# Kernel optimization log

Hardware: AMD Instinct MI355X
Metric: run time of the kernel (lower is better)

## Reference

```python
import jax, jax.numpy as jnp
import numpy as np

D_MODEL, N_HEADS, D_K, D_V = 512, 8, 32, 32
LN_EPS = 1e-5


def setup_inputs() -> dict:
    key = jax.random.key(0)
    ks = jax.random.split(key, 12)
    B, L = 4, 2048
    inner = N_HEADS * D_K
    s_in = 1.0 / np.sqrt(D_MODEL)
    s_fc = 1.0 / np.sqrt(inner)
    return {
        "q": jax.random.normal(ks[0], (B, L, D_MODEL), jnp.float32),
        "k": jax.random.normal(ks[1], (B, L, D_MODEL), jnp.float32),
        "v": jax.random.normal(ks[2], (B, L, D_MODEL), jnp.float32),
        "Wq": jax.random.normal(ks[3], (inner, D_MODEL), jnp.float32) * s_in,
        "bq": jax.random.normal(ks[4], (inner,), jnp.float32) * 0.01,
        "Wk": jax.random.normal(ks[5], (inner, D_MODEL), jnp.float32) * s_in,
        "bk": jax.random.normal(ks[6], (inner,), jnp.float32) * 0.01,
        "Wv": jax.random.normal(ks[7], (N_HEADS * D_V, D_MODEL), jnp.float32) * s_in,
        "bv": jax.random.normal(ks[8], (N_HEADS * D_V,), jnp.float32) * 0.01,
        "Wfc": jax.random.normal(ks[9], (D_MODEL, N_HEADS * D_V), jnp.float32) * s_fc,
        "bfc": jax.random.normal(ks[10], (D_MODEL,), jnp.float32) * 0.01,
        "gamma": jnp.ones((D_MODEL,), jnp.float32),
        "beta": jnp.zeros((D_MODEL,), jnp.float32),
    }


def reference(q, k, v, Wq, bq, Wk, bk, Wv, bv, Wfc, bfc, gamma, beta):
    n, l, _ = q.shape
    # Projection output interpreted as (..., d_k, n_heads): head idx is fastest dim
    def split_heads(x, W, b, dh):
        p = x @ W.T + b                     # [n, l, dh*H]
        return p.reshape(n, x.shape[1], dh, N_HEADS).transpose(0, 3, 1, 2)  # [n,H,l,dh]

    qh = split_heads(q, Wq, bq, D_K)
    kh = split_heads(k, Wk, bk, D_K)
    vh = split_heads(v, Wv, bv, D_V)

    scale = 1.0 / jnp.sqrt(jnp.asarray(D_K, q.dtype))
    scores = jnp.einsum('nhqd,nhkd->nhqk', qh, kh) * scale  # [n,H,L,L]
    att = jax.nn.softmax(scores, axis=-1)
    out = jnp.einsum('nhqk,nhkd->nhqd', att, vh)             # [n,H,L,d_v]
    out = out.transpose(0, 2, 1, 3).reshape(n, l, N_HEADS * D_V)

    fc = out @ Wfc.T + bfc
    x = fc + q  # residual
    mean = jnp.mean(x, axis=-1, keepdims=True)
    var = jnp.mean(jnp.square(x - mean), axis=-1, keepdims=True)
    return gamma * (x - mean) / jnp.sqrt(var + LN_EPS) + beta
```

## Files before the change

### kernel.cpp

```cpp
#include <hip/hip_runtime.h>
#include <math.h>

constexpr int Bn = 4, Ln = 2048, DM = 512, NH = 8, DKv = 32, INNER = 256;
constexpr int TTOK = Bn * Ln;
constexpr size_t HEAD_ELEMS = (size_t)Bn * NH * Ln * DKv;


typedef short short8 __attribute__((ext_vector_type(8)));
typedef short short4v __attribute__((ext_vector_type(4)));
typedef float floatx4 __attribute__((ext_vector_type(4)));

constexpr size_t XB_OFF  = 8u * 1024 * 1024;
constexpr size_t WB_OFF  = 12536832;
constexpr size_t WFCB_OFF = WB_OFF + 3 * 131072;

__device__ inline short f2bf(float x) {
  unsigned u = __builtin_bit_cast(unsigned, x);
  unsigned r = (u + 0x7FFFu + ((u >> 16) & 1u)) >> 16;
  return (short)r;
}

#if __has_builtin(__builtin_amdgcn_mfma_f32_16x16x16bf16_1k)
#define MFMA16(a, b, c) __builtin_amdgcn_mfma_f32_16x16x16bf16_1k(a, b, c, 0, 0, 0)
#else
__device__ inline floatx4 mfma16_asm(short4v a, short4v b, floatx4 c) {
  asm volatile("v_mfma_f32_16x16x16_bf16 %0, %1, %2, %3\n\ts_nop 4"
               : "=v"(c) : "v"(a), "v"(b), "0"(c));
  return c;
}
#define MFMA16(a, b, c) mfma16_asm(a, b, c)
#endif

__global__ __launch_bounds__(256) void cvtw_kernel(
    const float* __restrict__ Wq, const float* __restrict__ Wk,
    const float* __restrict__ Wv, const float* __restrict__ Wfc,
    short* __restrict__ Wb, short* __restrict__ Wfcb)
{
  const int z = blockIdx.y;
  const float* src = z == 0 ? Wq : (z == 1 ? Wk : (z == 2 ? Wv : Wfc));
  short* dst = z < 3 ? Wb + (size_t)z * 131072 : Wfcb;
  const int idx = (blockIdx.x * 256 + threadIdx.x) * 4;
  float4 x = *(const float4*)&src[idx];
  *(short4v*)&dst[idx] = (short4v){f2bf(x.x), f2bf(x.y), f2bf(x.z), f2bf(x.w)};
}

__global__ __launch_bounds__(256) void proj_kernel(
    const float* __restrict__ q, const float* __restrict__ k, const float* __restrict__ v,
    const short* __restrict__ Wb,
    const float* __restrict__ bq, const float* __restrict__ bk,
    const float* __restrict__ bv,
    short* __restrict__ ws)
{
  const int mat = blockIdx.z;
  const float* X    = mat == 0 ? q  : (mat == 1 ? k  : v);
  const short* W    = Wb + (size_t)mat * 131072;
  const float* bias = mat == 0 ? bq : (mat == 1 ? bk : bv);
  short* outp = ws + (size_t)mat * HEAD_ELEMS;

  const int t0 = blockIdx.x * 64;
  const int c0 = blockIdx.y * 64;
  const int tid = threadIdx.x;
  const int col = tid & 15;
  const int quad = (tid & 63) >> 4;
  const int w = tid >> 6;

  __shared__ short Xs[64 * 136];
  __shared__ short Wsh[64 * 136];

  floatx4 acc[4];
#pragma unroll
  for (int nj = 0; nj < 4; ++nj) acc[nj] = (floatx4){0.f, 0.f, 0.f, 0.f};

  float4 xr[8];
  short8 wr[4];
  auto loadX = [&](int k0) {
#pragma unroll
    for (int j = 0; j < 8; ++j) {
      const int i = tid + j * 256, row = i >> 5, c4 = i & 31;
      xr[j] = *(const float4*)&X[(size_t)(t0 + row) * DM + k0 + c4 * 4];
    }
  };
  auto loadW = [&](int k0) {
#pragma unroll
    for (int j = 0; j < 4; ++j) {
      const int s = tid + j * 256, row = s >> 4, k8 = s & 15;
      wr[j] = *(const short8*)&W[(size_t)(c0 + row) * DM + k0 + k8 * 8];
    }
  };

  loadX(0);
  loadW(0);

  for (int kc = 0; kc < 4; ++kc) {
#pragma unroll
    for (int j = 0; j < 8; ++j) {
      const int i = tid + j * 256, row = i >> 5, c4 = i & 31;
      *(short4v*)&Xs[row * 136 + c4 * 4] =
          (short4v){f2bf(xr[j].x), f2bf(xr[j].y), f2bf(xr[j].z), f2bf(xr[j].w)};
    }
#pragma unroll
    for (int j = 0; j < 4; ++j) {
      const int s = tid + j * 256, row = s >> 4, k8 = s & 15;
      *(short8*)&Wsh[row * 136 + k8 * 8] = wr[j];
    }
    __syncthreads();
    if (kc < 3) {
      loadX((kc + 1) * 128);
      loadW((kc + 1) * 128);
    }
#pragma unroll
    for (int ks = 0; ks < 4; ++ks) {
      short8 a = *(const short8*)&Xs[(w * 16 + col) * 136 + ks * 32 + quad * 8];
#pragma unroll
      for (int nj = 0; nj < 4; ++nj) {
        short8 b = *(const short8*)&Wsh[(nj * 16 + col) * 136 + ks * 32 + quad * 8];
        acc[nj] = __builtin_amdgcn_mfma_f32_16x16x32_bf16(a, b, acc[nj], 0, 0, 0);
      }
    }
    __syncthreads();
  }

#pragma unroll
  for (int nj = 0; nj < 4; ++nj) {
#pragma unroll
    for (int r = 0; r < 4; ++r) {
      const int t = t0 + w * 16 + quad * 4 + r;
      const int n = t >> 11, ll = t & (Ln - 1);
      const int c = c0 + nj * 16 + col;
      const int d = c >> 3, h = c & 7;
      const short val = f2bf(acc[nj][r] + bias[c]);
      if (mat < 2)
        outp[((size_t)(n * NH + h) * Ln + ll) * DKv + d] = val;
      else
        outp[((size_t)(n * NH + h) * DKv + d) * Ln + ll] = val;
    }
  }
}

__global__ __launch_bounds__(256) void attn_kernel(const short* __restrict__ ws,
                                                   short* __restrict__ O2b)
{
  const int bh = blockIdx.y;
  const int n = bh >> 3, h = bh & 7;
  const int tid = threadIdx.x;
  const int col = tid & 15;
  const int quad = (tid & 63) >> 4;
  const int w = tid >> 6;
  const int qi = blockIdx.x * 64 + w * 16 + col;

  const short* Qh = ws;
  const short* Kg = ws + HEAD_ELEMS + (size_t)bh * Ln * DKv;
  const short* Vg = ws + 2 * HEAD_ELEMS + (size_t)bh * DKv * Ln;

  __shared__ short Ks[64 * 32];
  __shared__ short Vs[32 * 72];

  const short8 aq = *(const short8*)&Qh[(size_t)bh * Ln * DKv + (size_t)qi * DKv + quad * 8];

  const float c1 = 0.25505654f;
  float lsum = 0.f;
  floatx4 o[2];
  o[0] = (floatx4){0.f, 0.f, 0.f, 0.f};
  o[1] = (floatx4){0.f, 0.f, 0.f, 0.f};

  const int vd = tid >> 3, vkb = tid & 7;
  short8 kr = *(const short8*)(Kg + tid * 8);
  short8 vr = *(const short8*)(Vg + (size_t)vd * Ln + vkb * 8);

  for (int kt = 0; kt < 32; ++kt) {
    *(short8*)&Ks[tid * 8] = kr;
    *(short8*)&Vs[vd * 72 + vkb * 8] = vr;
    __syncthreads();
    if (kt < 31) {
      kr = *(const short8*)(Kg + (size_t)(kt + 1) * 2048 + tid * 8);
      vr = *(const short8*)(Vg + (size_t)vd * Ln + (kt + 1) * 64 + vkb * 8);
    }

    floatx4 s[4];
    const floatx4 z4 = {0.f, 0.f, 0.f, 0.f};
#pragma unroll
    for (int ks = 0; ks < 4; ++ks) {
      short8 kf = *(const short8*)&Ks[(ks * 16 + col) * 32 + quad * 8];
      s[ks] = __builtin_amdgcn_mfma_f32_16x16x32_bf16(kf, aq, z4, 0, 0, 0);
    }

    short4v pf[4];
#pragma unroll
    for (int ks = 0; ks < 4; ++ks) {
      float p0 = __builtin_amdgcn_exp2f(s[ks][0] * c1);
      float p1 = __builtin_amdgcn_exp2f(s[ks][1] * c1);
      float p2 = __builtin_amdgcn_exp2f(s[ks][2] * c1);
      float p3 = __builtin_amdgcn_exp2f(s[ks][3] * c1);
      lsum += (p0 + p1) + (p2 + p3);
      unsigned u0 = __builtin_amdgcn_perm(__builtin_bit_cast(unsigned, p1),
                                          __builtin_bit_cast(unsigned, p0), 0x07060302u);
      unsigned u1 = __builtin_amdgcn_perm(__builtin_bit_cast(unsigned, p3),
                                          __builtin_bit_cast(unsigned, p2), 0x07060302u);
      uint2 uu = make_uint2(u0, u1);
      pf[ks] = __builtin_bit_cast(short4v, uu);
    }

#pragma unroll
    for (int ks = 0; ks < 4; ++ks) {
      short4v va0 = *(const short4v*)&Vs[col * 72 + ks * 16 + quad * 4];
      short4v va1 = *(const short4v*)&Vs[(16 + col) * 72 + ks * 16 + quad * 4];
      o[0] = MFMA16(va0, pf[ks], o[0]);
      o[1] = MFMA16(va1, pf[ks], o[1]);
    }
    __syncthreads();
  }

  lsum += __shfl_xor(lsum, 16);
  lsum += __shfl_xor(lsum, 32);
  const float inv = 1.f / lsum;

  short* dst = &O2b[((size_t)n * Ln + qi) * INNER + h * DKv];
#pragma unroll
  for (int dt = 0; dt < 2; ++dt)
#pragma unroll
    for (int r = 0; r < 4; ++r)
      dst[dt * 16 + quad * 4 + r] = f2bf(o[dt][r] * inv);
}

__global__ __launch_bounds__(256) void fc_kernel(
    const short* __restrict__ O2b, const short* __restrict__ Wfcb,
    const float* __restrict__ bfc, const float* __restrict__ qin,
    short* __restrict__ Xb)
{
  const int t0 = blockIdx.x * 64;
  const int c0 = blockIdx.y * 64;
  const int tid = threadIdx.x;
  const int col = tid & 15;
  const int quad = (tid & 63) >> 4;
  const int w = tid >> 6;

  __shared__ short As[64 * 264];
  __shared__ short Bs[64 * 264];

  for (int i = tid; i < 2048; i += 256) {
    const int row = i >> 5, k8 = i & 31;
    *(short8*)&As[row * 264 + k8 * 8] =
        *(const short8*)&O2b[(size_t)(t0 + row) * INNER + k8 * 8];
    *(short8*)&Bs[row * 264 + k8 * 8] =
        *(const short8*)&Wfcb[(size_t)(c0 + row) * INNER + k8 * 8];
  }
  __syncthreads();

  floatx4 acc[4];
#pragma unroll
  for (int nj = 0; nj < 4; ++nj) acc[nj] = (floatx4){0.f, 0.f, 0.f, 0.f};

#pragma unroll
  for (int ks = 0; ks < 8; ++ks) {
    short8 a = *(const short8*)&As[(w * 16 + col) * 264 + ks * 32 + quad * 8];
#pragma unroll
    for (int nj = 0; nj < 4; ++nj) {
      short8 b = *(const short8*)&Bs[(nj * 16 + col) * 264 + ks * 32 + quad * 8];
      acc[nj] = __builtin_amdgcn_mfma_f32_16x16x32_bf16(a, b, acc[nj], 0, 0, 0);
    }
  }

#pragma unroll
  for (int nj = 0; nj < 4; ++nj) {
#pragma unroll
    for (int r = 0; r < 4; ++r) {
      const int t = t0 + w * 16 + quad * 4 + r;
      const int c = c0 + nj * 16 + col;
      Xb[(size_t)t * DM + c] = f2bf(acc[nj][r] + bfc[c] + qin[(size_t)t * DM + c]);
    }
  }
}

__global__ __launch_bounds__(256) void ln_kernel(
    const short* __restrict__ Xb, const float* __restrict__ gamma,
    const float* __restrict__ beta, float* __restrict__ outp)
{
  const int t = blockIdx.x * 4 + (threadIdx.x >> 6);
  const int lane = threadIdx.x & 63;

  short8 xs = *(const short8*)&Xb[(size_t)t * DM + lane * 8];
  float x[8];
#pragma unroll
  for (int j = 0; j < 8; ++j)
    x[j] = __builtin_bit_cast(float, ((unsigned)(unsigned short)xs[j]) << 16);

  float s1 = 0.f, s2 = 0.f;
#pragma unroll
  for (int j = 0; j < 8; ++j) { s1 += x[j]; s2 += x[j] * x[j]; }
#pragma unroll
  for (int off = 32; off >= 1; off >>= 1) {
    s1 += __shfl_xor(s1, off);
    s2 += __shfl_xor(s2, off);
  }
  const float mean = s1 * (1.f / 512.f);
  const float var = s2 * (1.f / 512.f) - mean * mean;
  const float rstd = rsqrtf(var + 1e-5f);

  float4 g0 = *(const float4*)&gamma[lane * 8];
  float4 g1 = *(const float4*)&gamma[lane * 8 + 4];
  float4 b0 = *(const float4*)&beta[lane * 8];
  float4 b1 = *(const float4*)&beta[lane * 8 + 4];

  float4 y0, y1;
  y0.x = g0.x * (x[0] - mean) * rstd + b0.x;
  y0.y = g0.y * (x[1] - mean) * rstd + b0.y;
  y0.z = g0.z * (x[2] - mean) * rstd + b0.z;
  y0.w = g0.w * (x[3] - mean) * rstd + b0.w;
  y1.x = g1.x * (x[4] - mean) * rstd + b1.x;
  y1.y = g1.y * (x[5] - mean) * rstd + b1.y;
  y1.z = g1.z * (x[6] - mean) * rstd + b1.z;
  y1.w = g1.w * (x[7] - mean) * rstd + b1.w;

  float* drow = &outp[(size_t)t * DM + lane * 8];
  *(float4*)&drow[0] = y0;
  *(float4*)&drow[4] = y1;
}

extern "C" void kernel_launch(void* const* d_in, const int* in_sizes, int n_in,
                              void* d_out, int out_size, void* d_ws, size_t ws_size,
                              hipStream_t stream) {
  const float* q     = (const float*)d_in[0];
  const float* k     = (const float*)d_in[1];
  const float* v     = (const float*)d_in[2];
  const float* Wq    = (const float*)d_in[3];
  const float* bq    = (const float*)d_in[4];
  const float* Wk    = (const float*)d_in[5];
  const float* bk    = (const float*)d_in[6];
  const float* Wv    = (const float*)d_in[7];
  const float* bv    = (const float*)d_in[8];
  const float* Wfc   = (const float*)d_in[9];
  const float* bfc   = (const float*)d_in[10];
  const float* gamma = (const float*)d_in[11];
  const float* beta  = (const float*)d_in[12];

  short* wsS  = (short*)d_ws;
  short* O2b  = wsS + 3 * HEAD_ELEMS;
  short* Xb   = wsS + XB_OFF;
  short* Wb   = wsS + WB_OFF;
  short* Wfcb = wsS + WFCB_OFF;

  cvtw_kernel<<<dim3(128, 4), 256, 0, stream>>>(Wq, Wk, Wv, Wfc, Wb, Wfcb);

  dim3 gp(TTOK / 64, INNER / 64, 3);
  proj_kernel<<<gp, 256, 0, stream>>>(q, k, v, Wb, bq, bk, bv, wsS);

  dim3 gatt(Ln / 64, Bn * NH);
  attn_kernel<<<gatt, 256, 0, stream>>>(wsS, O2b);

  dim3 gfc(TTOK / 64, DM / 64);
  fc_kernel<<<gfc, 256, 0, stream>>>(O2b, Wfcb, bfc, q, Xb);

  ln_kernel<<<TTOK / 4, 256, 0, stream>>>(Xb, gamma, beta, (float*)d_out);
}
```

Baseline: 190.6 us.

## Double-buffer attention K/V tiles, pre-swizzle V in LDS, fold softmax scale into Q

The attention kernel now ping-pongs between two LDS buffers for K and V, which drops the trailing barrier in each tile iteration. V is written to shared memory in a permuted layout so each lane fetches both MFMA A-operands for a k-step with one 16-byte read. The softmax scale constant moves into the Q projection epilogue, removing a multiply per score. Pre-scaling Q before bf16 rounding changes numerics slightly, and the doubled LDS footprint may reduce occupancy.

```diff
diff --git a/kernel.cpp b/kernel.cpp
--- a/kernel.cpp
+++ b/kernel.cpp
@@ -13,6 +13,8 @@
 constexpr size_t XB_OFF  = 8u * 1024 * 1024;
 constexpr size_t WB_OFF  = 12536832;
 constexpr size_t WFCB_OFF = WB_OFF + 3 * 131072;
+
+constexpr float C1 = 0.25505654f;
 
 __device__ inline short f2bf(float x) {
   unsigned u = __builtin_bit_cast(unsigned, x);
@@ -128,7 +130,9 @@
       const int n = t >> 11, ll = t & (Ln - 1);
       const int c = c0 + nj * 16 + col;
       const int d = c >> 3, h = c & 7;
-      const short val = f2bf(acc[nj][r] + bias[c]);
+      float pv = acc[nj][r] + bias[c];
+      if (mat == 0) pv *= C1;
+      const short val = f2bf(pv);
       if (mat < 2)
         outp[((size_t)(n * NH + h) * Ln + ll) * DKv + d] = val;
       else
@@ -152,24 +156,29 @@
   const short* Kg = ws + HEAD_ELEMS + (size_t)bh * Ln * DKv;
   const short* Vg = ws + 2 * HEAD_ELEMS + (size_t)bh * DKv * Ln;
 
-  __shared__ short Ks[64 * 32];
-  __shared__ short Vs[32 * 72];
+  __shared__ short Ks[2][64 * 32];
+  __shared__ short Vs[2][64 * 32];
 
   const short8 aq = *(const short8*)&Qh[(size_t)bh * Ln * DKv + (size_t)qi * DKv + quad * 8];
 
-  const float c1 = 0.25505654f;
   float lsum = 0.f;
   floatx4 o[2];
   o[0] = (floatx4){0.f, 0.f, 0.f, 0.f};
   o[1] = (floatx4){0.f, 0.f, 0.f, 0.f};
 
   const int vd = tid >> 3, vkb = tid & 7;
+  const int voff1 = (vkb >> 1) * 512 + ((2 * vkb) & 3) * 128 + (vd & 15) * 8 + (vd >> 4) * 4;
+  const int voff2 = (vkb >> 1) * 512 + ((2 * vkb + 1) & 3) * 128 + (vd & 15) * 8 + (vd >> 4) * 4;
+
   short8 kr = *(const short8*)(Kg + tid * 8);
   short8 vr = *(const short8*)(Vg + (size_t)vd * Ln + vkb * 8);
 
   for (int kt = 0; kt < 32; ++kt) {
-    *(short8*)&Ks[tid * 8] = kr;
-    *(short8*)&Vs[vd * 72 + vkb * 8] = vr;
+    short* ksb = Ks[kt & 1];
+    short* vsb = Vs[kt & 1];
+    *(short8*)&ksb[tid * 8] = kr;
+    *(short4v*)&vsb[voff1] = __builtin_shufflevector(vr, vr, 0, 1, 2, 3);
+    *(short4v*)&vsb[voff2] = __builtin_shufflevector(vr, vr, 4, 5, 6, 7);
     __syncthreads();
     if (kt < 31) {
       kr = *(const short8*)(Kg + (size_t)(kt + 1) * 2048 + tid * 8);
@@ -180,17 +189,17 @@
     const floatx4 z4 = {0.f, 0.f, 0.f, 0.f};
 #pragma unroll
     for (int ks = 0; ks < 4; ++ks) {
-      short8 kf = *(const short8*)&Ks[(ks * 16 + col) * 32 + quad * 8];
+      short8 kf = *(const short8*)&ksb[(ks * 16 + col) * 32 + quad * 8];
       s[ks] = __builtin_amdgcn_mfma_f32_16x16x32_bf16(kf, aq, z4, 0, 0, 0);
     }
 
     short4v pf[4];
 #pragma unroll
     for (int ks = 0; ks < 4; ++ks) {
-      float p0 = __builtin_amdgcn_exp2f(s[ks][0] * c1);
-      float p1 = __builtin_amdgcn_exp2f(s[ks][1] * c1);
-      float p2 = __builtin_amdgcn_exp2f(s[ks][2] * c1);
-      float p3 = __builtin_amdgcn_exp2f(s[ks][3] * c1);
+      float p0 = __builtin_amdgcn_exp2f(s[ks][0]);
+      float p1 = __builtin_amdgcn_exp2f(s[ks][1]);
+      float p2 = __builtin_amdgcn_exp2f(s[ks][2]);
+      float p3 = __builtin_amdgcn_exp2f(s[ks][3]);
       lsum += (p0 + p1) + (p2 + p3);
       unsigned u0 = __builtin_amdgcn_perm(__builtin_bit_cast(unsigned, p1),
                                           __builtin_bit_cast(unsigned, p0), 0x07060302u);
@@ -202,12 +211,10 @@
 
 #pragma unroll
     for (int ks = 0; ks < 4; ++ks) {
-      short4v va0 = *(const short4v*)&Vs[col * 72 + ks * 16 + quad * 4];
-      short4v va1 = *(const short4v*)&Vs[(16 + col) * 72 + ks * 16 + quad * 4];
-      o[0] = MFMA16(va0, pf[ks], o[0]);
-      o[1] = MFMA16(va1, pf[ks], o[1]);
-    }
-    __syncthreads();
+      short8 vv = *(const short8*)&vsb[ks * 512 + quad * 128 + col * 8];
+      o[0] = MFMA16(__builtin_shufflevector(vv, vv, 0, 1, 2, 3), pf[ks], o[0]);
+      o[1] = MFMA16(__builtin_shufflevector(vv, vv, 4, 5, 6, 7), pf[ks], o[1]);
+    }
   }
 
   lsum += __shfl_xor(lsum, 16);
```

Measured after the change: 194.2 us. Within noise of the previous version (+1.9%).
